# Performance work log

Measured on AMD Instinct MI355X. Metric: run time of the kernel, lower is better.

## Reference

```python
import jax, jax.numpy as jnp
import numpy as np

K_BINS = 2048
EMB = 64
MU = 0.99
THRESHOLD = 1.0


def setup_inputs() -> dict:
    key = jax.random.key(0)
    kx, kk = jax.random.split(key)
    x = jax.random.normal(kx, (131072, EMB), dtype=jnp.float32)
    k = jax.random.normal(kk, (K_BINS, EMB), dtype=jnp.float32)
    # restore_k semantics: k_sum starts as a copy of k, k_elem as ones
    return {"x": x, "k": k, "k_sum": k, "k_elem": jnp.ones((K_BINS,), jnp.float32)}


def reference(x, k, k_sum, k_elem):
    N, T = x.shape  # T == EMB (preprocess branch 1)
    # preprocess: prenorm statistic
    prenorm = jnp.linalg.norm(x - jnp.mean(x)) / np.sqrt(x.size)

    # quantise: squared-L2 distance to codebook, argmin, fit
    dist = (jnp.sum(x * x, axis=-1, keepdims=True)
            - 2.0 * (x @ k.T)
            + jnp.sum(k * k, axis=-1)[None, :])  # (N, K_BINS)
    x_l = jnp.argmin(dist, axis=-1)               # (N,)
    fit = jnp.mean(jnp.min(dist, axis=-1))

    # dequantise: codebook gather
    x_d = k[x_l]                                  # (N, EMB)

    # update_k (torch.no_grad block): EMA codebook update
    _k_sum = jax.ops.segment_sum(x, x_l, num_segments=K_BINS)          # == onehot @ x
    _k_elem = jax.ops.segment_sum(jnp.ones((N,), x.dtype), x_l, num_segments=K_BINS)
    # N >= K_BINS so _tile is identity; randperm -> deterministic jax perm
    perm = jax.random.permutation(jax.random.key(42), N)
    _k_rand = x[perm[:K_BINS]]                    # (K_BINS, EMB)
    new_k_sum = MU * k_sum + (1.0 - MU) * _k_sum
    new_k_elem = MU * k_elem + (1.0 - MU) * _k_elem
    usage = (new_k_elem[:, None] >= THRESHOLD).astype(x.dtype)
    new_k = usage * (new_k_sum / new_k_elem[:, None]) + (1.0 - usage) * _k_rand
    _k_prob = _k_elem / jnp.sum(_k_elem)
    entropy = -jnp.sum(_k_prob * jnp.log(_k_prob + 1e-8))
    used_curr = jnp.sum((_k_elem >= THRESHOLD).astype(jnp.int32))
    usage_total = jnp.sum(usage)
    dk = jnp.linalg.norm(new_k - k) / np.sqrt(new_k.size)

    # commit loss (x_d detached) and straight-through estimator
    commit_loss = jnp.sum((jax.lax.stop_gradient(x_d) - x) ** 2) / x.size
    x_d_st = x + jax.lax.stop_gradient(x_d - x)

    # postprocess: view(N, T, -1).permute(0, 2, 1) -> (N, 1, EMB)
    x_d_out = x_d_st.reshape(N, T, -1).transpose(0, 2, 1)
    return (x_l, x_d_out, commit_loss, fit, prenorm,
            entropy, used_curr, usage_total, dk,
            new_k, new_k_sum, new_k_elem)
```

## Files before the change

kernel.cpp:

```cpp
#include <hip/hip_runtime.h>
#include <stdint.h>

#define N_ROWS 131072
#define DIM 64
#define KB 2048
#define M_ELEMS 8388608

#define O_XL   0
#define O_XD   131072
#define O_CL   8519680
#define O_FIT  8519681
#define O_PRE  8519682
#define O_ENT  8519683
#define O_USED 8519684
#define O_UTOT 8519685
#define O_DK   8519686
#define O_NK   8519687
#define O_NKS  8650759
#define O_NKE  8781831

#define A_DBL   0
#define A_CNT   64
#define A_KK2N  128
#define A_KST   8320
#define A_XLI   532608
#define A_KCNT  1056896
#define A_BCUR  1065088
#define A_KRAND 1073280
#define A_BOFF  1597568
#define A_FLAG  1605760
#define A_ROWL  2130048
#define A_KS64  2654336
#define A_BITS  1605760
#define A_PKEY  2130048
#define A_HIST  3702912
#define A_BSUM  3833984
#define A_CUR   3834496
#define A_PIDX  3965568
#define A_RES1  4489856
#define WS_END  5014144

typedef short bf16x8 __attribute__((ext_vector_type(8)));
typedef float f32x4 __attribute__((ext_vector_type(4)));

#define GLL16(G, L) __builtin_amdgcn_global_load_lds( \
    (const __attribute__((address_space(1))) void*)(G), \
    (__attribute__((address_space(3))) void*)(L), 16, 0, 0)
#define GLL4(G, L) __builtin_amdgcn_global_load_lds( \
    (const __attribute__((address_space(1))) void*)(G), \
    (__attribute__((address_space(3))) void*)(L), 4, 0, 0)


__device__ __forceinline__ float block_reduce_sum(float v, float* lds) {
  #pragma unroll
  for (int off = 32; off > 0; off >>= 1) v += __shfl_down(v, off, 64);
  int lane = threadIdx.x & 63, wid = threadIdx.x >> 6;
  if (lane == 0) lds[wid] = v;
  __syncthreads();
  float r = 0.f;
  if (threadIdx.x == 0) {
    int nw = blockDim.x >> 6;
    for (int i = 0; i < nw; ++i) r += lds[i];
  }
  __syncthreads();
  return r;
}

__device__ __forceinline__ unsigned short f2bf_rne(float f) {
  uint32_t u = __float_as_uint(f);
  uint32_t r = u + 0x7FFFu + ((u >> 16) & 1u);
  return (unsigned short)(r >> 16);
}

#define TF_ROUND(r) do { x0 += x1; x1 = (x1 << (r)) | (x1 >> (32 - (r))); x1 ^= x0; } while (0)

__device__ __forceinline__ void threefry2x32(uint32_t k0, uint32_t k1,
                                             uint32_t c0, uint32_t c1,
                                             uint32_t& o0, uint32_t& o1) {
  uint32_t k2 = k0 ^ k1 ^ 0x1BD11BDAu;
  uint32_t x0 = c0 + k0, x1 = c1 + k1;
  TF_ROUND(13); TF_ROUND(15); TF_ROUND(26); TF_ROUND(6);
  x0 += k1; x1 += k2 + 1u;
  TF_ROUND(17); TF_ROUND(29); TF_ROUND(16); TF_ROUND(24);
  x0 += k2; x1 += k0 + 2u;
  TF_ROUND(13); TF_ROUND(15); TF_ROUND(26); TF_ROUND(6);
  x0 += k0; x1 += k1 + 3u;
  TF_ROUND(17); TF_ROUND(29); TF_ROUND(16); TF_ROUND(24);
  x0 += k1; x1 += k2 + 4u;
  TF_ROUND(13); TF_ROUND(15); TF_ROUND(26); TF_ROUND(6);
  x0 += k2; x1 += k0 + 5u;
  o0 = x0; o1 = x1;
}

__global__ __launch_bounds__(256) void k_prep(
    const float* __restrict__ k, unsigned short* __restrict__ kst,
    float* __restrict__ kk2n) {
  int w = (blockIdx.x * blockDim.x + threadIdx.x) >> 6;
  int lane = threadIdx.x & 63;
  float v = k[(size_t)w * DIM + lane];
  unsigned short h = f2bf_rne(v);
  float hf = __uint_as_float((uint32_t)h << 16);
  unsigned short lo = f2bf_rne(v - hf);
  int t = w >> 4, r = w & 15;
  int c = lane >> 3, e = lane & 7;
  int slot = c ^ (r & 7);
  size_t u16i = (size_t)t * 2048 + r * 64 + slot * 8 + e;
  kst[u16i] = h;
  kst[u16i + 1024] = lo;
  float q = v * v;
  #pragma unroll
  for (int off = 32; off > 0; off >>= 1) q += __shfl_down(q, off, 64);
  if (lane == 0) kk2n[w] = -0.5f * q;
}

__global__ __launch_bounds__(256) void k_main(
    const float* __restrict__ x, const unsigned short* __restrict__ kst,
    const float* __restrict__ kk2n,
    int* __restrict__ xli, uint32_t* __restrict__ flag, int* __restrict__ cnt,
    double* __restrict__ dbl) {
  __shared__ __align__(16) char smem[2][16640];
  __shared__ float lds_red[4];
  int tid = threadIdx.x;
  int lane = tid & 63;
  int wid = tid >> 6;
  int lrow = lane & 15;
  int lk = lane >> 4;
  int r0 = (blockIdx.x * 4 + wid) * 64;

  bf16x8 xh[4][2], xl[4][2];
  float s_acc = 0.f, q_acc = 0.f;
  #pragma unroll
  for (int g = 0; g < 4; ++g) {
    #pragma unroll
    for (int kt = 0; kt < 2; ++kt) {
      const float* xp = x + (size_t)(r0 + g * 16 + lrow) * DIM + kt * 32 + lk * 8;
      float4 v0 = *(const float4*)xp;
      float4 v1 = *(const float4*)(xp + 4);
      float vv[8] = {v0.x, v0.y, v0.z, v0.w, v1.x, v1.y, v1.z, v1.w};
      #pragma unroll
      for (int i = 0; i < 8; ++i) {
        float v = vv[i];
        s_acc += v;
        q_acc = fmaf(v, v, q_acc);
        unsigned short h = f2bf_rne(v);
        float hf = __uint_as_float((uint32_t)h << 16);
        xh[g][kt][i] = (short)h;
        xl[g][kt][i] = (short)f2bf_rne(v - hf);
      }
    }
  }
  float bs = block_reduce_sum(s_acc, lds_red);
  float bq = block_reduce_sum(q_acc, lds_red);
  if (tid == 0) {
    atomicAdd(&dbl[0], (double)bs);
    atomicAdd(&dbl[1], (double)bq);
  }

  int offH0 = lrow * 128 + (((lk    ) ^ (lrow & 7)) << 4);
  int offH1 = lrow * 128 + (((lk + 4) ^ (lrow & 7)) << 4);

  const char* kst_b = (const char*)kst;
  const char* kk_b  = (const char*)kk2n;

  {
    char* ldst = &smem[0][0];
    #pragma unroll
    for (int c = 0; c < 4; ++c)
      GLL16(kst_b + c * 4096 + tid * 16, ldst + c * 4096 + tid * 16);
    if (wid == 0) GLL4(kk_b + lane * 4, ldst + 16384 + lane * 4);
  }

  float b1[4], b2[4];
  uint32_t j1[4];
  #pragma unroll
  for (int g = 0; g < 4; ++g) {
    b1[g] = -3.402823466e38f; b2[g] = -3.402823466e38f; j1[g] = 0;
  }

  for (int t = 0; t < 32; ++t) {
    __syncthreads();
    if (t + 1 < 32) {
      const char* gsrc = kst_b + (size_t)(t + 1) * 16384;
      char* ldst = &smem[(t + 1) & 1][0];
      #pragma unroll
      for (int c = 0; c < 4; ++c)
        GLL16(gsrc + c * 4096 + tid * 16, ldst + c * 4096 + tid * 16);
      if (wid == 0) GLL4(kk_b + (size_t)(t + 1) * 256 + lane * 4, ldst + 16384 + lane * 4);
    }
    const char* B = &smem[t & 1][0];
    #pragma unroll
    for (int s = 0; s < 4; ++s) {
      bf16x8 ah0 = *(const bf16x8*)(B + s * 4096 + offH0);
      bf16x8 ah1 = *(const bf16x8*)(B + s * 4096 + offH1);
      bf16x8 al0 = *(const bf16x8*)(B + s * 4096 + 2048 + offH0);
      bf16x8 al1 = *(const bf16x8*)(B + s * 4096 + 2048 + offH1);
      f32x4 kkv  = *(const f32x4*)(B + 16384 + s * 64 + lk * 16);
      uint32_t jb = (uint32_t)(t * 64 + s * 16 + lk * 4);
      #pragma unroll
      for (int g = 0; g < 4; ++g) {
        f32x4 acc = __builtin_amdgcn_mfma_f32_16x16x32_bf16(ah0, xh[g][0], kkv, 0, 0, 0);
        acc = __builtin_amdgcn_mfma_f32_16x16x32_bf16(ah1, xh[g][1], acc, 0, 0, 0);
        acc = __builtin_amdgcn_mfma_f32_16x16x32_bf16(al0, xh[g][0], acc, 0, 0, 0);
        acc = __builtin_amdgcn_mfma_f32_16x16x32_bf16(al1, xh[g][1], acc, 0, 0, 0);
        acc = __builtin_amdgcn_mfma_f32_16x16x32_bf16(ah0, xl[g][0], acc, 0, 0, 0);
        acc = __builtin_amdgcn_mfma_f32_16x16x32_bf16(ah1, xl[g][1], acc, 0, 0, 0);
        #pragma unroll
        for (int reg = 0; reg < 4; ++reg) {
          float v = acc[reg];
          bool gt = v > b1[g];
          float mn = fminf(v, b1[g]);
          b2[g] = fmaxf(b2[g], mn);
          b1[g] = gt ? v : b1[g];
          j1[g] = gt ? (jb + (uint32_t)reg) : j1[g];
        }
      }
    }
  }

  #pragma unroll
  for (int g = 0; g < 4; ++g) {
    #pragma unroll
    for (int s = 16; s <= 32; s <<= 1) {
      float ob1 = __shfl_xor(b1[g], s, 64);
      float ob2 = __shfl_xor(b2[g], s, 64);
      uint32_t oj1 = __shfl_xor(j1[g], s, 64);
      bool gt = ob1 > b1[g];
      float mn = fminf(b1[g], ob1);
      b2[g] = fmaxf(fmaxf(b2[g], ob2), mn);
      b1[g] = fmaxf(b1[g], ob1);
      j1[g] = gt ? oj1 : j1[g];
    }
    if (lk == 0) {
      int row = r0 + g * 16 + lrow;
      xli[row] = (int)j1[g];
      if (b1[g] - b2[g] < 0.01f) {
        int i = atomicAdd(cnt, 1);
        flag[i] = (uint32_t)row;
      }
    }
  }
}

__global__ __launch_bounds__(256) void k_rescan(
    const uint32_t* __restrict__ flag, const int* __restrict__ cnt,
    const float* __restrict__ x, const float* __restrict__ k,
    int* __restrict__ xli) {
  __shared__ float xs[4][64];
  int lane = threadIdx.x & 63;
  int wid = threadIdx.x >> 6;
  int gw = (blockIdx.x * blockDim.x + threadIdx.x) >> 6;
  int n = *cnt;
  for (int fi = gw; fi < n; fi += 1024) {
    int row = flag[fi];
    xs[wid][lane] = x[(size_t)row * DIM + lane];
    double bd = 1e300;
    int bj = 0;
    for (int j = lane; j < KB; j += 64) {
      const float* kr = k + (size_t)j * DIM;
      double e = 0.0;
      #pragma unroll
      for (int d = 0; d < DIM; ++d) {
        double diff = (double)xs[wid][d] - (double)kr[d];
        e = fma(diff, diff, e);
      }
      if (e < bd) { bd = e; bj = j; }
    }
    #pragma unroll
    for (int off = 32; off > 0; off >>= 1) {
      double od = __shfl_down(bd, off, 64);
      int oj = __shfl_down(bj, off, 64);
      if (od < bd || (od == bd && oj < bj)) { bd = od; bj = oj; }
    }
    if (lane == 0) xli[row] = bj;
  }
}

__global__ void k_hist_rows(const int* __restrict__ xli, int* __restrict__ kcnt) {
  int i = blockIdx.x * blockDim.x + threadIdx.x;
  atomicAdd(&kcnt[xli[i]], 1);
}

__global__ __launch_bounds__(256) void k_finish(
    const float* __restrict__ x, const float* __restrict__ k,
    const int* __restrict__ xli, float* __restrict__ out,
    double* __restrict__ dbl) {
  __shared__ float lds[8];
  int row = blockIdx.x * blockDim.x + threadIdx.x;
  int j = xli[row];
  out[O_XL + row] = (float)j;
  const float4* xp = (const float4*)(x + (size_t)row * DIM);
  const float4* kp = (const float4*)(k + (size_t)j * DIM);
  float4* xd = (float4*)(out + O_XD + (size_t)row * DIM);
  float a = 0.f, b = 0.f, c = 0.f, d = 0.f;
  #pragma unroll
  for (int q = 0; q < 16; ++q) {
    float4 kv = kp[q];
    float4 xv = xp[q];
    xd[q] = kv;
    float dx = kv.x - xv.x, dy = kv.y - xv.y;
    float dz = kv.z - xv.z, dw = kv.w - xv.w;
    a = fmaf(dx, dx, a); b = fmaf(dy, dy, b);
    c = fmaf(dz, dz, c); d = fmaf(dw, dw, d);
  }
  float cl = (a + b) + (c + d);
  float bc = block_reduce_sum(cl, lds);
  if (threadIdx.x == 0) atomicAdd(&dbl[2], (double)bc);
}


__global__ __launch_bounds__(1024) void k_scan_bins(const int* __restrict__ kcnt,
                                                    uint32_t* __restrict__ boffs) {
  __shared__ uint32_t part[1024];
  int tid = threadIdx.x;
  uint32_t c0 = (uint32_t)kcnt[2 * tid];
  uint32_t c1 = (uint32_t)kcnt[2 * tid + 1];
  part[tid] = c0 + c1;
  __syncthreads();
  for (int off = 1; off < 1024; off <<= 1) {
    uint32_t v = (tid >= off) ? part[tid - off] : 0u;
    __syncthreads();
    part[tid] += v;
    __syncthreads();
  }
  uint32_t run = (tid > 0) ? part[tid - 1] : 0u;
  boffs[2 * tid] = run;
  boffs[2 * tid + 1] = run + c0;
}

__global__ void k_scatter_rows(const int* __restrict__ xli, const uint32_t* __restrict__ boffs,
                               uint32_t* __restrict__ bcur, uint32_t* __restrict__ rowlist) {
  int i = blockIdx.x * blockDim.x + threadIdx.x;
  int b = xli[i];
  uint32_t pos = boffs[b] + atomicAdd(&bcur[b], 1u);
  rowlist[pos] = (uint32_t)i;
}

__global__ __launch_bounds__(256) void k_segsum(
    const uint32_t* __restrict__ rowlist, const int* __restrict__ xli,
    const float* __restrict__ x, double* __restrict__ ks64) {
  int gw = (blockIdx.x * blockDim.x + threadIdx.x) >> 6;
  int lane = threadIdx.x & 63;
  uint32_t p0 = (uint32_t)gw * 16;
  double acc = 0.0;
  int cur = -1;
  #pragma unroll 4
  for (int i = 0; i < 16; ++i) {
    uint32_t row = rowlist[p0 + i];
    int bin = xli[row];
    if (bin != cur) {
      if (cur >= 0) atomicAdd(&ks64[(size_t)cur * DIM + lane], acc);
      acc = 0.0; cur = bin;
    }
    acc += (double)x[(size_t)row * DIM + lane];
  }
  if (cur >= 0) atomicAdd(&ks64[(size_t)cur * DIM + lane], acc);
}


__global__ void k_bits_hist(int which, uint32_t* __restrict__ bits,
                            uint32_t* __restrict__ hist) {
  uint32_t a0, a1, b0, b1;
  threefry2x32(0u, 42u, 0u, 2u, a0, b0);
  threefry2x32(0u, 42u, 1u, 3u, a1, b1);
  uint32_t k0, k1;
  if (which == 0) { k0 = b0; k1 = b1; }
  else {
    uint32_t c0, c1, d0, d1;
    threefry2x32(a0, a1, 0u, 2u, c0, d0);
    threefry2x32(a0, a1, 1u, 3u, c1, d1);
    k0 = d0; k1 = d1;
  }
  int i = blockIdx.x * blockDim.x + threadIdx.x;
  uint32_t y0, y1;
  threefry2x32(k0, k1, (uint32_t)i, (uint32_t)(i + 65536), y0, y1);
  bits[i] = y0;
  bits[i + 65536] = y1;
  atomicAdd(&hist[y0 >> 17], 1u);
  atomicAdd(&hist[y1 >> 17], 1u);
}

__global__ __launch_bounds__(256) void k_scanA(uint32_t* __restrict__ hist,
                                               uint32_t* __restrict__ bsum) {
  __shared__ uint32_t sh[256];
  int tid = threadIdx.x;
  int bin = blockIdx.x * 256 + tid;
  uint32_t v = hist[bin];
  sh[tid] = v;
  __syncthreads();
  for (int off = 1; off < 256; off <<= 1) {
    uint32_t t = (tid >= off) ? sh[tid - off] : 0u;
    __syncthreads();
    sh[tid] += t;
    __syncthreads();
  }
  hist[bin] = sh[tid] - v;
  if (tid == 255) bsum[blockIdx.x] = sh[tid];
}

__global__ void k_scanB(uint32_t* __restrict__ bsum) {
  __shared__ uint32_t sh[128];
  int tid = threadIdx.x;
  uint32_t v = bsum[tid];
  sh[tid] = v;
  __syncthreads();
  for (int off = 1; off < 128; off <<= 1) {
    uint32_t t = (tid >= off) ? sh[tid - off] : 0u;
    __syncthreads();
    sh[tid] += t;
    __syncthreads();
  }
  bsum[tid] = sh[tid] - v;
}

__global__ void k_scatter(const uint32_t* __restrict__ bits, const uint32_t* __restrict__ hist,
                          const uint32_t* __restrict__ bsum, uint32_t* __restrict__ cursor,
                          uint32_t* __restrict__ pkey, uint32_t* __restrict__ pidx) {
  int i = blockIdx.x * blockDim.x + threadIdx.x;
  uint32_t key = bits[i];
  uint32_t bin = key >> 17;
  uint32_t pos = hist[bin] + bsum[bin >> 8] + atomicAdd(&cursor[bin], 1u);
  pkey[pos] = key; pidx[pos] = (uint32_t)i;
}

__global__ void k_rank(const uint32_t* __restrict__ pkey, const uint32_t* __restrict__ pidx,
                       const uint32_t* __restrict__ hist, const uint32_t* __restrict__ bsum,
                       const uint32_t* __restrict__ cursor,
                       const uint32_t* __restrict__ srcvals, uint32_t* __restrict__ outv,
                       const float* __restrict__ x, float* __restrict__ krand,
                       int limit) {
  int s = blockIdx.x * blockDim.x + threadIdx.x;
  uint32_t myk = pkey[s], myi = pidx[s];
  uint32_t bin = myk >> 17;
  uint32_t start = hist[bin] + bsum[bin >> 8], cntb = cursor[bin];
  uint32_t r = 0;
  for (uint32_t t = 0; t < cntb; ++t) {
    uint32_t ok = pkey[start + t], oi = pidx[start + t];
    r += (ok < myk || (ok == myk && oi < myi)) ? 1u : 0u;
  }
  uint32_t pos = start + r;
  if (limit == 0) {
    outv[pos] = myi;
  } else if (pos < (uint32_t)limit) {
    uint32_t orig = srcvals[myi];
    const float4* xs = (const float4*)(x + (size_t)orig * DIM);
    float4* kd = (float4*)(krand + (size_t)pos * DIM);
    #pragma unroll
    for (int q = 0; q < 16; ++q) kd[q] = xs[q];
  }
}


__global__ __launch_bounds__(256) void k_elem_kernel(
    const double* __restrict__ ks64, const int* __restrict__ kcnt,
    const float* __restrict__ k_sum_in, const float* __restrict__ k_elem_in,
    const float* __restrict__ k_in, const float* __restrict__ krand,
    float* __restrict__ out, double* __restrict__ dbl) {
  __shared__ float lds[8];
  const float OMF = (float)(1.0 - 0.99);
  int e = blockIdx.x * blockDim.x + threadIdx.x;
  int b = e >> 6;
  float part = (float)ks64[e];
  float nks = 0.99f * k_sum_in[e] + OMF * part;
  out[O_NKS + e] = nks;
  float cnt = (float)kcnt[b];
  float ke = 0.99f * k_elem_in[b] + OMF * cnt;
  float nk = (ke >= 1.f) ? (nks / ke) : krand[e];
  out[O_NK + e] = nk;
  float dd = nk - k_in[e];
  float bsum = block_reduce_sum(dd * dd, lds);
  if (threadIdx.x == 0) atomicAdd(&dbl[4], (double)bsum);
}

__global__ __launch_bounds__(1024) void k_finale(
    const int* __restrict__ kcnt, const float* __restrict__ k_elem_in,
    float* __restrict__ out, const double* __restrict__ dbl) {
  __shared__ float ent_l[1024];
  __shared__ int u1_l[1024], u2_l[1024];
  const float OMF = (float)(1.0 - 0.99);
  int tid = threadIdx.x;
  float ent = 0.f; int used = 0, usage = 0;
  #pragma unroll
  for (int t = 0; t < 2; ++t) {
    int b = tid + t * 1024;
    float cnt = (float)kcnt[b];
    float ke = 0.99f * k_elem_in[b] + OMF * cnt;
    out[O_NKE + b] = ke;
    float p = cnt * (1.f / 131072.f);
    ent -= p * logf(p + 1e-8f);
    used += (cnt >= 1.f) ? 1 : 0;
    usage += (ke >= 1.f) ? 1 : 0;
  }
  ent_l[tid] = ent; u1_l[tid] = used; u2_l[tid] = usage;
  __syncthreads();
  for (int off = 512; off > 0; off >>= 1) {
    if (tid < off) {
      ent_l[tid] += ent_l[tid + off];
      u1_l[tid] += u1_l[tid + off];
      u2_l[tid] += u2_l[tid + off];
    }
    __syncthreads();
  }
  if (tid == 0) {
    double M = (double)M_ELEMS;
    double sumS = dbl[0], sumQ = dbl[1];
    double var = (sumQ - sumS * sumS / M) / M;
    out[O_PRE] = (float)sqrt(var > 0.0 ? var : 0.0);
    out[O_FIT] = (float)(dbl[2] / (double)N_ROWS);
    out[O_CL]  = (float)(dbl[2] / M);
    out[O_DK]  = (float)sqrt(dbl[4] / (double)(KB * DIM));
    out[O_ENT] = ent_l[0];
    out[O_USED] = (float)u1_l[0];
    out[O_UTOT] = (float)u2_l[0];
  }
}


extern "C" void kernel_launch(void* const* d_in, const int* in_sizes, int n_in,
                              void* d_out, int out_size, void* d_ws, size_t ws_size,
                              hipStream_t stream) {
  (void)in_sizes; (void)n_in; (void)out_size; (void)ws_size;
  const float* x      = (const float*)d_in[0];
  const float* k      = (const float*)d_in[1];
  const float* k_sum  = (const float*)d_in[2];
  const float* k_elem = (const float*)d_in[3];
  float* out = (float*)d_out;
  char* ws = (char*)d_ws;

  double*   dbl   = (double*)(ws + A_DBL);
  int*      cnt   = (int*)(ws + A_CNT);
  float*    kk2n  = (float*)(ws + A_KK2N);
  unsigned short* kst = (unsigned short*)(ws + A_KST);
  int*      xli   = (int*)(ws + A_XLI);
  int*      kcnt  = (int*)(ws + A_KCNT);
  uint32_t* bcur  = (uint32_t*)(ws + A_BCUR);
  float*    krand = (float*)(ws + A_KRAND);
  uint32_t* boffs = (uint32_t*)(ws + A_BOFF);
  uint32_t* flag  = (uint32_t*)(ws + A_FLAG);
  uint32_t* rowl  = (uint32_t*)(ws + A_ROWL);
  double*   ks64  = (double*)(ws + A_KS64);
  uint32_t* bits  = (uint32_t*)(ws + A_BITS);
  uint32_t* pkey  = (uint32_t*)(ws + A_PKEY);
  uint32_t* hist  = (uint32_t*)(ws + A_HIST);
  uint32_t* bsum  = (uint32_t*)(ws + A_BSUM);
  uint32_t* cur   = (uint32_t*)(ws + A_CUR);
  uint32_t* pidx  = (uint32_t*)(ws + A_PIDX);
  uint32_t* res1  = (uint32_t*)(ws + A_RES1);

  (void)hipMemsetAsync(ws + A_DBL, 0, 128, stream);
  (void)hipMemsetAsync(ws + A_KCNT, 0, 16384, stream);
  (void)hipMemsetAsync(ws + A_KS64, 0, 1048576, stream);

  k_prep<<<512, 256, 0, stream>>>(k, kst, kk2n);
  k_main<<<512, 256, 0, stream>>>(x, kst, kk2n, xli, flag, cnt, dbl);
  k_rescan<<<256, 256, 0, stream>>>(flag, cnt, x, k, xli);
  k_finish<<<512, 256, 0, stream>>>(x, k, xli, out, dbl);

  k_hist_rows<<<512, 256, 0, stream>>>(xli, kcnt);
  k_scan_bins<<<1, 1024, 0, stream>>>(kcnt, boffs);
  k_scatter_rows<<<512, 256, 0, stream>>>(xli, boffs, bcur, rowl);
  k_segsum<<<2048, 256, 0, stream>>>(rowl, xli, x, ks64);

  (void)hipMemsetAsync(ws + A_HIST, 0, 262656, stream);
  k_bits_hist<<<256, 256, 0, stream>>>(0, bits, hist);
  k_scanA<<<128, 256, 0, stream>>>(hist, bsum);
  k_scanB<<<1, 128, 0, stream>>>(bsum);
  k_scatter<<<512, 256, 0, stream>>>(bits, hist, bsum, cur, pkey, pidx);
  k_rank<<<512, 256, 0, stream>>>(pkey, pidx, hist, bsum, cur, nullptr, res1,
                                  nullptr, nullptr, 0);
  (void)hipMemsetAsync(ws + A_HIST, 0, 262656, stream);
  k_bits_hist<<<256, 256, 0, stream>>>(1, bits, hist);
  k_scanA<<<128, 256, 0, stream>>>(hist, bsum);
  k_scanB<<<1, 128, 0, stream>>>(bsum);
  k_scatter<<<512, 256, 0, stream>>>(bits, hist, bsum, cur, pkey, pidx);
  k_rank<<<512, 256, 0, stream>>>(pkey, pidx, hist, bsum, cur, res1, nullptr,
                                  x, krand, 2048);

  k_elem_kernel<<<512, 256, 0, stream>>>(ks64, kcnt, k_sum, k_elem, k, krand, out, dbl);
  k_finale<<<1, 1024, 0, stream>>>(kcnt, k_elem, out, dbl);
}
```

Measured before the change: 385.3 us.

## Fuse dequantise gather and commit loss into distance kernel, halve rows per wave

The separate finish kernel is removed. The main distance kernel now writes the gathered codebook rows, the float index output and a commit-loss partial computed algebraically as ||x||^2 - 2*best score. The rescan kernel rewrites the outputs and corrects the loss only for rows whose argmin changes. Rows per wave drop from 64 to 32 and the grid doubles to 1024 blocks, which lowers register use and raises parallelism but loads each codebook tile twice as often. The algebraic loss goes through bf16-split MFMA scores and may differ slightly from the direct sum of squared differences.

```diff
diff --git a/kernel.cpp b/kernel.cpp
--- a/kernel.cpp
+++ b/kernel.cpp
@@ -114,10 +114,10 @@
 }
 
 __global__ __launch_bounds__(256) void k_main(
-    const float* __restrict__ x, const unsigned short* __restrict__ kst,
-    const float* __restrict__ kk2n,
+    const float* __restrict__ x, const float* __restrict__ korig,
+    const unsigned short* __restrict__ kst, const float* __restrict__ kk2n,
     int* __restrict__ xli, uint32_t* __restrict__ flag, int* __restrict__ cnt,
-    double* __restrict__ dbl) {
+    float* __restrict__ out, double* __restrict__ dbl) {
   __shared__ __align__(16) char smem[2][16640];
   __shared__ float lds_red[4];
   int tid = threadIdx.x;
@@ -125,12 +125,13 @@
   int wid = tid >> 6;
   int lrow = lane & 15;
   int lk = lane >> 4;
-  int r0 = (blockIdx.x * 4 + wid) * 64;
-
-  bf16x8 xh[4][2], xl[4][2];
-  float s_acc = 0.f, q_acc = 0.f;
+  int r0 = (blockIdx.x * 4 + wid) * 32;
+
+  bf16x8 xh[2][2], xl[2][2];
+  float qrow[2] = {0.f, 0.f};
+  float s_acc = 0.f;
   #pragma unroll
-  for (int g = 0; g < 4; ++g) {
+  for (int g = 0; g < 2; ++g) {
     #pragma unroll
     for (int kt = 0; kt < 2; ++kt) {
       const float* xp = x + (size_t)(r0 + g * 16 + lrow) * DIM + kt * 32 + lk * 8;
@@ -141,7 +142,7 @@
       for (int i = 0; i < 8; ++i) {
         float v = vv[i];
         s_acc += v;
-        q_acc = fmaf(v, v, q_acc);
+        qrow[g] = fmaf(v, v, qrow[g]);
         unsigned short h = f2bf_rne(v);
         float hf = __uint_as_float((uint32_t)h << 16);
         xh[g][kt][i] = (short)h;
@@ -150,7 +151,7 @@
     }
   }
   float bs = block_reduce_sum(s_acc, lds_red);
-  float bq = block_reduce_sum(q_acc, lds_red);
+  float bq = block_reduce_sum(qrow[0] + qrow[1], lds_red);
   if (tid == 0) {
     atomicAdd(&dbl[0], (double)bs);
     atomicAdd(&dbl[1], (double)bq);
@@ -170,10 +171,10 @@
     if (wid == 0) GLL4(kk_b + lane * 4, ldst + 16384 + lane * 4);
   }
 
-  float b1[4], b2[4];
-  uint32_t j1[4];
+  float b1[2], b2[2];
+  uint32_t j1[2];
   #pragma unroll
-  for (int g = 0; g < 4; ++g) {
+  for (int g = 0; g < 2; ++g) {
     b1[g] = -3.402823466e38f; b2[g] = -3.402823466e38f; j1[g] = 0;
   }
 
@@ -197,7 +198,7 @@
       f32x4 kkv  = *(const f32x4*)(B + 16384 + s * 64 + lk * 16);
       uint32_t jb = (uint32_t)(t * 64 + s * 16 + lk * 4);
       #pragma unroll
-      for (int g = 0; g < 4; ++g) {
+      for (int g = 0; g < 2; ++g) {
         f32x4 acc = __builtin_amdgcn_mfma_f32_16x16x32_bf16(ah0, xh[g][0], kkv, 0, 0, 0);
         acc = __builtin_amdgcn_mfma_f32_16x16x32_bf16(ah1, xh[g][1], acc, 0, 0, 0);
         acc = __builtin_amdgcn_mfma_f32_16x16x32_bf16(al0, xh[g][0], acc, 0, 0, 0);
@@ -217,34 +218,47 @@
     }
   }
 
+  float cl_acc = 0.f;
   #pragma unroll
-  for (int g = 0; g < 4; ++g) {
+  for (int g = 0; g < 2; ++g) {
+    float xxr = qrow[g];
     #pragma unroll
     for (int s = 16; s <= 32; s <<= 1) {
       float ob1 = __shfl_xor(b1[g], s, 64);
       float ob2 = __shfl_xor(b2[g], s, 64);
       uint32_t oj1 = __shfl_xor(j1[g], s, 64);
+      xxr += __shfl_xor(xxr, s, 64);
       bool gt = ob1 > b1[g];
       float mn = fminf(b1[g], ob1);
       b2[g] = fmaxf(fmaxf(b2[g], ob2), mn);
       b1[g] = fmaxf(b1[g], ob1);
       j1[g] = gt ? oj1 : j1[g];
     }
+    int row = r0 + g * 16 + lrow;
+    {
+      const float4* kp = (const float4*)(korig + (size_t)j1[g] * DIM + lk * 16);
+      float4* xd = (float4*)(out + O_XD + (size_t)row * DIM + lk * 16);
+      #pragma unroll
+      for (int q = 0; q < 4; ++q) xd[q] = kp[q];
+    }
     if (lk == 0) {
-      int row = r0 + g * 16 + lrow;
       xli[row] = (int)j1[g];
+      out[O_XL + row] = (float)j1[g];
+      cl_acc += fmaf(-2.f, b1[g], xxr);
       if (b1[g] - b2[g] < 0.01f) {
         int i = atomicAdd(cnt, 1);
         flag[i] = (uint32_t)row;
       }
     }
   }
+  float bc = block_reduce_sum(cl_acc, lds_red);
+  if (tid == 0) atomicAdd(&dbl[2], (double)bc);
 }
 
 __global__ __launch_bounds__(256) void k_rescan(
     const uint32_t* __restrict__ flag, const int* __restrict__ cnt,
     const float* __restrict__ x, const float* __restrict__ k,
-    int* __restrict__ xli) {
+    int* __restrict__ xli, float* __restrict__ out, double* __restrict__ dbl) {
   __shared__ float xs[4][64];
   int lane = threadIdx.x & 63;
   int wid = threadIdx.x >> 6;
@@ -252,8 +266,10 @@
   int n = *cnt;
   for (int fi = gw; fi < n; fi += 1024) {
     int row = flag[fi];
+    int jold = xli[row];
     xs[wid][lane] = x[(size_t)row * DIM + lane];
     double bd = 1e300;
+    double eold = 0.0;
     int bj = 0;
     for (int j = lane; j < KB; j += 64) {
       const float* kr = k + (size_t)j * DIM;
@@ -264,47 +280,30 @@
         e = fma(diff, diff, e);
       }
       if (e < bd) { bd = e; bj = j; }
+      if (j == jold) eold = e;
     }
     #pragma unroll
     for (int off = 32; off > 0; off >>= 1) {
       double od = __shfl_down(bd, off, 64);
       int oj = __shfl_down(bj, off, 64);
+      eold += __shfl_down(eold, off, 64);
       if (od < bd || (od == bd && oj < bj)) { bd = od; bj = oj; }
     }
-    if (lane == 0) xli[row] = bj;
+    int bjf = __shfl(bj, 0, 64);
+    if (bjf != jold) {
+      out[O_XD + (size_t)row * DIM + lane] = k[(size_t)bjf * DIM + lane];
+      if (lane == 0) {
+        xli[row] = bjf;
+        out[O_XL + row] = (float)bjf;
+        atomicAdd(&dbl[2], bd - eold);
+      }
+    }
   }
 }
 
 __global__ void k_hist_rows(const int* __restrict__ xli, int* __restrict__ kcnt) {
   int i = blockIdx.x * blockDim.x + threadIdx.x;
   atomicAdd(&kcnt[xli[i]], 1);
-}
-
-__global__ __launch_bounds__(256) void k_finish(
-    const float* __restrict__ x, const float* __restrict__ k,
-    const int* __restrict__ xli, float* __restrict__ out,
-    double* __restrict__ dbl) {
-  __shared__ float lds[8];
-  int row = blockIdx.x * blockDim.x + threadIdx.x;
-  int j = xli[row];
-  out[O_XL + row] = (float)j;
-  const float4* xp = (const float4*)(x + (size_t)row * DIM);
-  const float4* kp = (const float4*)(k + (size_t)j * DIM);
-  float4* xd = (float4*)(out + O_XD + (size_t)row * DIM);
-  float a = 0.f, b = 0.f, c = 0.f, d = 0.f;
-  #pragma unroll
-  for (int q = 0; q < 16; ++q) {
-    float4 kv = kp[q];
-    float4 xv = xp[q];
-    xd[q] = kv;
-    float dx = kv.x - xv.x, dy = kv.y - xv.y;
-    float dz = kv.z - xv.z, dw = kv.w - xv.w;
-    a = fmaf(dx, dx, a); b = fmaf(dy, dy, b);
-    c = fmaf(dz, dz, c); d = fmaf(dw, dw, d);
-  }
-  float cl = (a + b) + (c + d);
-  float bc = block_reduce_sum(cl, lds);
-  if (threadIdx.x == 0) atomicAdd(&dbl[2], (double)bc);
 }
 
 
@@ -551,9 +550,8 @@
   (void)hipMemsetAsync(ws + A_KS64, 0, 1048576, stream);
 
   k_prep<<<512, 256, 0, stream>>>(k, kst, kk2n);
-  k_main<<<512, 256, 0, stream>>>(x, kst, kk2n, xli, flag, cnt, dbl);
-  k_rescan<<<256, 256, 0, stream>>>(flag, cnt, x, k, xli);
-  k_finish<<<512, 256, 0, stream>>>(x, k, xli, out, dbl);
+  k_main<<<1024, 256, 0, stream>>>(x, k, kst, kk2n, xli, flag, cnt, out, dbl);
+  k_rescan<<<256, 256, 0, stream>>>(flag, cnt, x, k, xli, out, dbl);
 
   k_hist_rows<<<512, 256, 0, stream>>>(xli, kcnt);
   k_scan_bins<<<1, 1024, 0, stream>>>(kcnt, boffs);
```

Result: faster. 374.6 us (-2.8%).
